# Performance work log

Hardware: AMD Instinct MI355X
Metric: run time of the kernel (lower is better)

Reference implementation:

```python
import jax, jax.numpy as jnp
import numpy as np

B, S, E, H = 2, 2048, 1024, 16
DH = E // H  # 64


def setup_inputs() -> dict:
    key = jax.random.key(0)
    ks = jax.random.split(key, 9)
    scale = 1.0 / np.sqrt(E)
    q = jax.random.normal(ks[0], (B, S, E), jnp.float32)
    k = jax.random.normal(ks[1], (B, S, E), jnp.float32)
    v = jax.random.normal(ks[2], (B, S, E), jnp.float32)
    Wq = jax.random.uniform(ks[3], (E, E), jnp.float32, -scale, scale)
    Wk = jax.random.uniform(ks[4], (E, E), jnp.float32, -scale, scale)
    Wv = jax.random.uniform(ks[5], (E, E), jnp.float32, -scale, scale)
    bq = jax.random.uniform(ks[6], (E,), jnp.float32, -scale, scale)
    bk = jax.random.uniform(ks[7], (E,), jnp.float32, -scale, scale)
    bv = jax.random.uniform(ks[8], (E,), jnp.float32, -scale, scale)
    # causal mask: True = masked. [b, s_q, s_k]
    causal = jnp.triu(jnp.ones((S, S), bool), k=1)
    mask = jnp.broadcast_to(causal, (B, S, S))
    return {"q": q, "k": k, "v": v, "Wq": Wq, "bq": bq, "Wk": Wk,
            "bk": bk, "Wv": Wv, "bv": bv, "mask": mask}


def reference(q, k, v, Wq, bq, Wk, bk, Wv, bv, mask):
    b, s_q, _ = q.shape
    s_k = k.shape[1]
    # NB: faithful to the original: .view(b, heads, s, -1) (no transpose)
    Q = (q @ Wq + bq).reshape(b, H, s_q, DH)
    K = (k @ Wk + bk).reshape(b, H, s_k, DH)
    V = (v @ Wv + bv).reshape(b, H, s_k, DH)
    scores = jnp.einsum('bhqd,bhkd->bhqk', Q, K) / jnp.sqrt(
        jnp.asarray(DH, Q.dtype))
    scores = jnp.where(mask[:, None, :, :], -jnp.inf, scores)
    attn = jax.nn.softmax(scores, axis=-1)
    out = jnp.einsum('bhqk,bhkd->bhqd', attn, V).reshape(b, s_q, -1)
    return out  # dropout p=0 / eval mode -> identity
```

## Files before the change

kernel.cpp:

```cpp
#include <hip/hip_runtime.h>

typedef unsigned short u16;
typedef __attribute__((ext_vector_type(8))) __bf16 bf16x8;
typedef __attribute__((ext_vector_type(4))) __bf16 bf16x4;
typedef __attribute__((ext_vector_type(4))) float f32x4;

#define MFMA(a, b, c) __builtin_amdgcn_mfma_f32_16x16x32_bf16((a), (b), (c), 0, 0, 0)
#define KSCALE 0.18033688011112042f

__device__ __forceinline__ void load_lds16(const void* g, void* l) {
  __builtin_amdgcn_global_load_lds(
      (__attribute__((address_space(1))) void*)(g),
      (__attribute__((address_space(3))) void*)(l), 16, 0, 0);
}

__device__ __forceinline__ float launder(float x, float lim) {
  return fminf(fmaxf(x, -lim), lim);
}

__global__ __launch_bounds__(256) void prep(
    const float* __restrict__ x0, const float* __restrict__ x1,
    const float* __restrict__ x2, const float* __restrict__ W0,
    const float* __restrict__ W1, const float* __restrict__ W2,
    __bf16* __restrict__ Xb, __bf16* __restrict__ WT) {
  __shared__ __bf16 tile[64][65];
  int bx = blockIdx.x;
  int t = threadIdx.x;
  if (bx < 3072) {
    int z = bx >> 10, blk = bx & 1023;
    const float* x = z == 0 ? x0 : (z == 1 ? x1 : x2);
    __bf16* o = Xb + (size_t)z * 4194304;
#pragma unroll
    for (int i = 0; i < 4; ++i) {
      size_t e = ((size_t)i * 262144 + (size_t)blk * 256 + t) * 4;
      f32x4 v = *(const f32x4*)&x[e];
      bf16x4 b = {(__bf16)v[0], (__bf16)v[1], (__bf16)v[2], (__bf16)v[3]};
      *(bf16x4*)&o[e] = b;
    }
  } else {
    int idx = bx - 3072;
    int z = idx >> 8, rest = idx & 255;
    const float* W = z == 0 ? W0 : (z == 1 ? W1 : W2);
    float sc = z == 0 ? KSCALE : 1.0f;
    __bf16* out = WT + (size_t)z * 1048576;
    int r0 = (rest >> 4) * 64, c0 = (rest & 15) * 64;
#pragma unroll
    for (int it = 0; it < 16; ++it) {
      int flat = it * 256 + t, r = flat >> 6, c = flat & 63;
      tile[c][r] = (__bf16)(W[(size_t)(r0 + r) * 1024 + c0 + c] * sc);
    }
    __syncthreads();
#pragma unroll
    for (int it = 0; it < 16; ++it) {
      int flat = it * 256 + t, r = flat >> 6, c = flat & 63;
      out[(size_t)(c0 + r) * 1024 + r0 + c] = tile[r][c];
    }
  }
}

__device__ __forceinline__ void pg_stage(
    const __bf16* __restrict__ A, const __bf16* __restrict__ Bm, int k0,
    __bf16* As, __bf16* Bs, int tid) {
#pragma unroll
  for (int r = 0; r < 2; ++r) {
    int flat = r * 256 + tid;
    load_lds16(A + (size_t)(flat >> 2) * 1024 + k0 + (flat & 3) * 8, &As[flat * 8]);
  }
#pragma unroll
  for (int r = 0; r < 2; ++r) {
    int flat = r * 256 + tid;
    load_lds16(Bm + (size_t)(flat >> 2) * 1024 + k0 + (flat & 3) * 8, &Bs[flat * 8]);
  }
}

__global__ __launch_bounds__(256, 3) void proj_gemm(
    const __bf16* __restrict__ Xb, const __bf16* __restrict__ WT,
    const float* __restrict__ bq, const float* __restrict__ bk,
    const float* __restrict__ bv, __bf16* __restrict__ QKV) {
  __shared__ __attribute__((aligned(16))) __bf16 As[2][4096];
  __shared__ __attribute__((aligned(16))) __bf16 Bs[2][4096];

  int tid = threadIdx.x;
  int lane = tid & 63, quad = lane >> 4, l16 = lane & 15;
  int w = tid >> 6;
  int wm = (w >> 1) * 64, wn = (w & 1) * 64;
  int m0 = blockIdx.x * 128;
  int z = m0 >> 12;
  int n0 = blockIdx.y * 128;
  const __bf16* A = Xb + (size_t)m0 * 1024;
  const __bf16* Bm = WT + (size_t)z * 1048576 + (size_t)n0 * 1024;

  f32x4 zero4 = {0.f, 0.f, 0.f, 0.f};
  f32x4 acc[4][4];
#pragma unroll
  for (int i = 0; i < 4; ++i)
#pragma unroll
    for (int j = 0; j < 4; ++j) acc[i][j] = zero4;

  pg_stage(A, Bm, 0, As[0], Bs[0], tid);

  for (int i = 0; i < 32; ++i) {
    int cur = i & 1;
    if (i < 31) {
      pg_stage(A, Bm, (i + 1) * 32, As[cur ^ 1], Bs[cur ^ 1], tid);
      asm volatile("s_waitcnt vmcnt(4)" ::: "memory");
    } else {
      asm volatile("s_waitcnt vmcnt(0)" ::: "memory");
    }
    __builtin_amdgcn_sched_barrier(0);
    __builtin_amdgcn_s_barrier();
    __builtin_amdgcn_sched_barrier(0);

    bf16x8 a[4], b[4];
#pragma unroll
    for (int mf = 0; mf < 4; ++mf)
      a[mf] = *(const bf16x8*)&As[cur][(wm + mf * 16 + l16) * 32 + quad * 8];
#pragma unroll
    for (int nf = 0; nf < 4; ++nf)
      b[nf] = *(const bf16x8*)&Bs[cur][(wn + nf * 16 + l16) * 32 + quad * 8];
#pragma unroll
    for (int mf = 0; mf < 4; ++mf)
#pragma unroll
      for (int nf = 0; nf < 4; ++nf) acc[mf][nf] = MFMA(a[mf], b[nf], acc[mf][nf]);

    __builtin_amdgcn_sched_barrier(0);
    __builtin_amdgcn_s_barrier();
    __builtin_amdgcn_sched_barrier(0);
  }

  int mrow = m0 & 4095;
  const float* bp = z == 0 ? bq : (z == 1 ? bk : bv);
  float bsc = z == 0 ? KSCALE : 1.0f;
  __bf16* O = QKV + (size_t)z * 4194304;
#pragma unroll
  for (int nf = 0; nf < 4; ++nf) {
    int n = n0 + wn + nf * 16 + l16;
    float bb = bp[n] * bsc;
#pragma unroll
    for (int mf = 0; mf < 4; ++mf) {
#pragma unroll
      for (int r = 0; r < 4; ++r) {
        int m = mrow + wm + mf * 16 + quad * 4 + r;
        O[(size_t)m * 1024 + n] = (__bf16)launder(acc[mf][nf][r] + bb, 512.f);
      }
    }
  }
}

__global__ __launch_bounds__(256) void transpose_v(
    const u16* __restrict__ Vp, u16* __restrict__ Vt) {
  int bh = blockIdx.y, s0 = blockIdx.x * 64;
  __shared__ u16 tile[64][65];
  int t = threadIdx.x;
  const u16* src = Vp + (size_t)bh * 131072;
  u16* dst = Vt + (size_t)bh * 131072;
#pragma unroll
  for (int it = 0; it < 16; ++it) {
    int flat = it * 256 + t, r = flat >> 6, d = flat & 63;
    tile[d][r] = src[(size_t)(s0 + r) * 64 + d];
  }
  __syncthreads();
#pragma unroll
  for (int it = 0; it < 16; ++it) {
    int flat = it * 256 + t, d = flat >> 6, c = flat & 63;
    dst[(size_t)d * 2048 + s0 + c] = tile[d][c];
  }
}

__global__ __launch_bounds__(256, 2) void flash_attn(
    const __bf16* __restrict__ Qp, const __bf16* __restrict__ Kp,
    const __bf16* __restrict__ Vt, float* __restrict__ out) {
  int qtA = blockIdx.x;
  int qtB = 31 - qtA;
  int bh = blockIdx.y;
  int t = threadIdx.x;
  int lane = t & 63, quad = lane >> 4, l16 = lane & 15;
  int w = t >> 6;
  int jmaxA = qtA >> 1, jmaxB = qtB >> 1;
  int sw = (l16 >> 1) & 3;

  __shared__ __attribute__((aligned(16))) __bf16 Ks[2][8192];
  __shared__ __attribute__((aligned(16))) __bf16 Vs[2][8192];
  __shared__ __attribute__((aligned(16))) __bf16 Ps[4][2048];

  const __bf16* Qb = Qp + (size_t)bh * 131072;
  const __bf16* Kb = Kp + (size_t)bh * 131072;
  const __bf16* Vb = Vt + (size_t)bh * 131072;
  __bf16* Pw = Ps[w];

  int qbA = qtA * 64 + w * 16, qbB = qtB * 64 + w * 16;

  bf16x8 qfA[2], qfB[2], ones;
#pragma unroll
  for (int i = 0; i < 8; ++i) ones[i] = (__bf16)1.0f;
#pragma unroll
  for (int kk = 0; kk < 2; ++kk) {
    qfA[kk] = *(const bf16x8*)&Qb[(size_t)(qbA + l16) * 64 + kk * 32 + quad * 8];
    qfB[kk] = *(const bf16x8*)&Qb[(size_t)(qbB + l16) * 64 + kk * 32 + quad * 8];
  }

  f32x4 zero4 = {0.f, 0.f, 0.f, 0.f};
  f32x4 oA[4], oB[4], lAacc = zero4, lBacc = zero4;
#pragma unroll
  for (int nd = 0; nd < 4; ++nd) { oA[nd] = zero4; oB[nd] = zero4; }

  int ks_kpos[4], ks_off[4], vs_d[4], vs_off[4], vs_kq[4];
#pragma unroll
  for (int p = 0; p < 4; ++p) {
    int c = p * 256 + t;
    int swz = ((c & 3) ^ ((c >> 3) & 3)) * 8;
    ks_kpos[p] = (c & 511) >> 2;
    ks_off[p] = (c >> 9) * 32 + swz;
    vs_kq[p] = c >> 8;
    vs_d[p] = (c & 255) >> 2;
    vs_off[p] = swz;
  }

  bf16x8 pk[4], pv[4];
#pragma unroll
  for (int p = 0; p < 4; ++p) {
    pk[p] = *(const bf16x8*)&Kb[(size_t)ks_kpos[p] * 64 + ks_off[p]];
    pv[p] = *(const bf16x8*)&Vb[(size_t)vs_d[p] * 2048 + vs_kq[p] * 32 + vs_off[p]];
  }
#pragma unroll
  for (int p = 0; p < 4; ++p) {
    int c = p * 256 + t;
    *(bf16x8*)&Ks[0][c * 8] = pk[p];
    *(bf16x8*)&Vs[0][c * 8] = pv[p];
  }
  if (jmaxB > 0) {
#pragma unroll
    for (int p = 0; p < 4; ++p) {
      pk[p] = *(const bf16x8*)&Kb[(size_t)(128 + ks_kpos[p]) * 64 + ks_off[p]];
      pv[p] = *(const bf16x8*)&Vb[(size_t)vs_d[p] * 2048 + 128 + vs_kq[p] * 32 + vs_off[p]];
    }
  }
  __syncthreads();

  for (int j = 0; j <= jmaxB; ++j) {
    int cur = j & 1, nxt = cur ^ 1;
    bool doA = (j <= jmaxA);

    if (j < jmaxB) {
#pragma unroll
      for (int p = 0; p < 4; ++p) {
        int c = p * 256 + t;
        *(bf16x8*)&Ks[nxt][c * 8] = pk[p];
        *(bf16x8*)&Vs[nxt][c * 8] = pv[p];
      }
      if (j + 1 < jmaxB) {
        int jn = (j + 2) * 128;
#pragma unroll
        for (int p = 0; p < 4; ++p) {
          pk[p] = *(const bf16x8*)&Kb[(size_t)(jn + ks_kpos[p]) * 64 + ks_off[p]];
          pv[p] = *(const bf16x8*)&Vb[(size_t)vs_d[p] * 2048 + jn + vs_kq[p] * 32 + vs_off[p]];
        }
      }
    }

    f32x4 sA[8], sB[8];
#pragma unroll
    for (int nt = 0; nt < 8; ++nt) {
      bf16x8 k0 = *(const bf16x8*)&Ks[cur][(nt * 16 + l16) * 32 + (quad ^ sw) * 8];
      bf16x8 k1 = *(const bf16x8*)&Ks[cur][4096 + (nt * 16 + l16) * 32 + (quad ^ sw) * 8];
      f32x4 zb = zero4;
      zb = MFMA(k0, qfB[0], zb);
      zb = MFMA(k1, qfB[1], zb);
      sB[nt] = zb;
      if (doA) {
        f32x4 za = zero4;
        za = MFMA(k0, qfA[0], za);
        za = MFMA(k1, qfA[1], za);
        sA[nt] = za;
      }
    }

    if (j == jmaxB) {
      int qg = qbB + l16;
#pragma unroll
      for (int nt = 0; nt < 8; ++nt) {
        int kg = j * 128 + nt * 16 + quad * 4;
#pragma unroll
        for (int r = 0; r < 4; ++r)
          if (kg + r > qg) sB[nt][r] = -1e30f;
      }
    }
#pragma unroll
    for (int nt = 0; nt < 8; ++nt) {
      bf16x4 pb;
#pragma unroll
      for (int r = 0; r < 4; ++r)
        pb[r] = (__bf16)__builtin_amdgcn_exp2f(sB[nt][r]);
      *(bf16x4*)&Pw[l16 * 128 + (((nt * 4 + quad) ^ (l16 * 2)) & 31) * 4] = pb;
    }
    {
      bf16x8 pf[4];
#pragma unroll
      for (int kk = 0; kk < 4; ++kk)
        pf[kk] = *(const bf16x8*)&Pw[l16 * 128 + (((kk * 8 + quad * 2) ^ (l16 * 2)) & 31) * 4];
#pragma unroll
      for (int kk = 0; kk < 4; ++kk) {
        lBacc = MFMA(ones, pf[kk], lBacc);
#pragma unroll
        for (int nd = 0; nd < 4; ++nd) {
          bf16x8 av = *(const bf16x8*)&Vs[cur][kk * 2048 + (nd * 16 + l16) * 32 + (quad ^ sw) * 8];
          oB[nd] = MFMA(av, pf[kk], oB[nd]);
        }
      }
    }

    if (doA) {
      if (j == jmaxA) {
        int qg = qbA + l16;
#pragma unroll
        for (int nt = 0; nt < 8; ++nt) {
          int kg = j * 128 + nt * 16 + quad * 4;
#pragma unroll
          for (int r = 0; r < 4; ++r)
            if (kg + r > qg) sA[nt][r] = -1e30f;
        }
      }
#pragma unroll
      for (int nt = 0; nt < 8; ++nt) {
        bf16x4 pb;
#pragma unroll
        for (int r = 0; r < 4; ++r)
          pb[r] = (__bf16)__builtin_amdgcn_exp2f(sA[nt][r]);
        *(bf16x4*)&Pw[l16 * 128 + (((nt * 4 + quad) ^ (l16 * 2)) & 31) * 4] = pb;
      }
      bf16x8 pf[4];
#pragma unroll
      for (int kk = 0; kk < 4; ++kk)
        pf[kk] = *(const bf16x8*)&Pw[l16 * 128 + (((kk * 8 + quad * 2) ^ (l16 * 2)) & 31) * 4];
#pragma unroll
      for (int kk = 0; kk < 4; ++kk) {
        lAacc = MFMA(ones, pf[kk], lAacc);
#pragma unroll
        for (int nd = 0; nd < 4; ++nd) {
          bf16x8 av = *(const bf16x8*)&Vs[cur][kk * 2048 + (nd * 16 + l16) * 32 + (quad ^ sw) * 8];
          oA[nd] = MFMA(av, pf[kk], oA[nd]);
        }
      }
    }
    __syncthreads();
  }

  {
    float invA = 1.f / lAacc[0], invB = 1.f / lBacc[0];
    int qA = qbA + l16, qB = qbB + l16;
#pragma unroll
    for (int nd = 0; nd < 4; ++nd) {
      f32x4 a, b;
#pragma unroll
      for (int r = 0; r < 4; ++r) {
        a[r] = launder(oA[nd][r] * invA, 512.f);
        b[r] = launder(oB[nd][r] * invB, 512.f);
      }
      *(f32x4*)&out[(size_t)bh * 131072 + (size_t)qA * 64 + nd * 16 + quad * 4] = a;
      *(f32x4*)&out[(size_t)bh * 131072 + (size_t)qB * 64 + nd * 16 + quad * 4] = b;
    }
  }
}

extern "C" void kernel_launch(void* const* d_in, const int* in_sizes, int n_in,
                              void* d_out, int out_size, void* d_ws, size_t ws_size,
                              hipStream_t stream) {
  (void)in_sizes; (void)n_in; (void)out_size; (void)ws_size;
  const float* q  = (const float*)d_in[0];
  const float* k  = (const float*)d_in[1];
  const float* v  = (const float*)d_in[2];
  const float* Wq = (const float*)d_in[3];
  const float* bq = (const float*)d_in[4];
  const float* Wk = (const float*)d_in[5];
  const float* bk = (const float*)d_in[6];
  const float* Wv = (const float*)d_in[7];
  const float* bv = (const float*)d_in[8];

  __bf16* ws  = (__bf16*)d_ws;
  __bf16* WT  = ws;
  __bf16* QKV = ws + (size_t)3 * 1048576;
  __bf16* Qp  = QKV;
  __bf16* Kp  = QKV + (size_t)4194304;
  __bf16* Vp  = QKV + (size_t)2 * 4194304;
  __bf16* Xb  = QKV + (size_t)3 * 4194304;
  __bf16* Vtr = Xb;

  prep<<<dim3(3840), 256, 0, stream>>>(q, k, v, Wq, Wk, Wv, Xb, WT);
  proj_gemm<<<dim3(96, 8), 256, 0, stream>>>(Xb, WT, bq, bk, bv, QKV);
  transpose_v<<<dim3(32, 32), 256, 0, stream>>>((const u16*)Vp, (u16*)Vtr);
  flash_attn<<<dim3(16, 32), 256, 0, stream>>>(Qp, Kp, Vtr, (float*)d_out);
}
```

Measured before the change: 210.5 us.

## Split paired-tile flash attention into single 64-row tiles with 64-key blocks

The flash attention kernel stops pairing two query tiles per block for causal load balancing. Each block now handles one 64-row query tile with 64-key KV blocks, on a grid of 32x32 blocks with a permuted tile order. Shared memory per block is halved and launch bounds are raised to allow 4 blocks per CU. This aims for higher occupancy and more blocks in flight, at the cost of more per-block overhead, more barriers per unit of work, and relying on the hardware scheduler for causal load balance.

```diff
diff --git a/kernel.cpp b/kernel.cpp
--- a/kernel.cpp
+++ b/kernel.cpp
@@ -167,197 +167,150 @@
   }
 }
 
-__global__ __launch_bounds__(256, 2) void flash_attn(
+__global__ __launch_bounds__(256, 4) void flash_attn(
     const __bf16* __restrict__ Qp, const __bf16* __restrict__ Kp,
     const __bf16* __restrict__ Vt, float* __restrict__ out) {
-  int qtA = blockIdx.x;
-  int qtB = 31 - qtA;
-  int bh = blockIdx.y;
+  int bh = blockIdx.x;
+  int yy = blockIdx.y;
+  int qt = (yy & 24) | (((yy >> 3) & 1) ? (7 - (yy & 7)) : (yy & 7));
+  int jmax = qt;
   int t = threadIdx.x;
   int lane = t & 63, quad = lane >> 4, l16 = lane & 15;
   int w = t >> 6;
-  int jmaxA = qtA >> 1, jmaxB = qtB >> 1;
   int sw = (l16 >> 1) & 3;
 
-  __shared__ __attribute__((aligned(16))) __bf16 Ks[2][8192];
-  __shared__ __attribute__((aligned(16))) __bf16 Vs[2][8192];
-  __shared__ __attribute__((aligned(16))) __bf16 Ps[4][2048];
+  __shared__ __attribute__((aligned(16))) __bf16 Ks[2][4096];
+  __shared__ __attribute__((aligned(16))) __bf16 Vs[2][4096];
+  __shared__ __attribute__((aligned(16))) __bf16 Ps[4][1024];
 
   const __bf16* Qb = Qp + (size_t)bh * 131072;
   const __bf16* Kb = Kp + (size_t)bh * 131072;
   const __bf16* Vb = Vt + (size_t)bh * 131072;
   __bf16* Pw = Ps[w];
 
-  int qbA = qtA * 64 + w * 16, qbB = qtB * 64 + w * 16;
-
-  bf16x8 qfA[2], qfB[2], ones;
+  int qb = qt * 64 + w * 16;
+
+  bf16x8 qf[2], ones;
 #pragma unroll
   for (int i = 0; i < 8; ++i) ones[i] = (__bf16)1.0f;
 #pragma unroll
-  for (int kk = 0; kk < 2; ++kk) {
-    qfA[kk] = *(const bf16x8*)&Qb[(size_t)(qbA + l16) * 64 + kk * 32 + quad * 8];
-    qfB[kk] = *(const bf16x8*)&Qb[(size_t)(qbB + l16) * 64 + kk * 32 + quad * 8];
-  }
+  for (int kk = 0; kk < 2; ++kk)
+    qf[kk] = *(const bf16x8*)&Qb[(size_t)(qb + l16) * 64 + kk * 32 + quad * 8];
 
   f32x4 zero4 = {0.f, 0.f, 0.f, 0.f};
-  f32x4 oA[4], oB[4], lAacc = zero4, lBacc = zero4;
-#pragma unroll
-  for (int nd = 0; nd < 4; ++nd) { oA[nd] = zero4; oB[nd] = zero4; }
-
-  int ks_kpos[4], ks_off[4], vs_d[4], vs_off[4], vs_kq[4];
-#pragma unroll
-  for (int p = 0; p < 4; ++p) {
+  f32x4 o[4], lacc = zero4;
+#pragma unroll
+  for (int nd = 0; nd < 4; ++nd) o[nd] = zero4;
+
+  int kq_row[2], kq_off[2], v_d[2], v_off[2], v_kk[2];
+#pragma unroll
+  for (int p = 0; p < 2; ++p) {
     int c = p * 256 + t;
     int swz = ((c & 3) ^ ((c >> 3) & 3)) * 8;
-    ks_kpos[p] = (c & 511) >> 2;
-    ks_off[p] = (c >> 9) * 32 + swz;
-    vs_kq[p] = c >> 8;
-    vs_d[p] = (c & 255) >> 2;
-    vs_off[p] = swz;
-  }
-
-  bf16x8 pk[4], pv[4];
-#pragma unroll
-  for (int p = 0; p < 4; ++p) {
-    pk[p] = *(const bf16x8*)&Kb[(size_t)ks_kpos[p] * 64 + ks_off[p]];
-    pv[p] = *(const bf16x8*)&Vb[(size_t)vs_d[p] * 2048 + vs_kq[p] * 32 + vs_off[p]];
-  }
-#pragma unroll
-  for (int p = 0; p < 4; ++p) {
+    kq_row[p] = (c & 255) >> 2;
+    kq_off[p] = (c >> 8) * 32 + swz;
+    v_kk[p] = c >> 8;
+    v_d[p] = (c & 255) >> 2;
+    v_off[p] = swz;
+  }
+
+  bf16x8 pk[2], pv[2];
+#pragma unroll
+  for (int p = 0; p < 2; ++p) {
+    pk[p] = *(const bf16x8*)&Kb[(size_t)kq_row[p] * 64 + kq_off[p]];
+    pv[p] = *(const bf16x8*)&Vb[(size_t)v_d[p] * 2048 + v_kk[p] * 32 + v_off[p]];
+  }
+#pragma unroll
+  for (int p = 0; p < 2; ++p) {
     int c = p * 256 + t;
     *(bf16x8*)&Ks[0][c * 8] = pk[p];
     *(bf16x8*)&Vs[0][c * 8] = pv[p];
   }
-  if (jmaxB > 0) {
-#pragma unroll
-    for (int p = 0; p < 4; ++p) {
-      pk[p] = *(const bf16x8*)&Kb[(size_t)(128 + ks_kpos[p]) * 64 + ks_off[p]];
-      pv[p] = *(const bf16x8*)&Vb[(size_t)vs_d[p] * 2048 + 128 + vs_kq[p] * 32 + vs_off[p]];
+  if (jmax > 0) {
+#pragma unroll
+    for (int p = 0; p < 2; ++p) {
+      pk[p] = *(const bf16x8*)&Kb[(size_t)(64 + kq_row[p]) * 64 + kq_off[p]];
+      pv[p] = *(const bf16x8*)&Vb[(size_t)v_d[p] * 2048 + 64 + v_kk[p] * 32 + v_off[p]];
     }
   }
   __syncthreads();
 
-  for (int j = 0; j <= jmaxB; ++j) {
+  for (int j = 0; j <= jmax; ++j) {
     int cur = j & 1, nxt = cur ^ 1;
-    bool doA = (j <= jmaxA);
-
-    if (j < jmaxB) {
-#pragma unroll
-      for (int p = 0; p < 4; ++p) {
+
+    if (j < jmax) {
+#pragma unroll
+      for (int p = 0; p < 2; ++p) {
         int c = p * 256 + t;
         *(bf16x8*)&Ks[nxt][c * 8] = pk[p];
         *(bf16x8*)&Vs[nxt][c * 8] = pv[p];
       }
-      if (j + 1 < jmaxB) {
-        int jn = (j + 2) * 128;
-#pragma unroll
-        for (int p = 0; p < 4; ++p) {
-          pk[p] = *(const bf16x8*)&Kb[(size_t)(jn + ks_kpos[p]) * 64 + ks_off[p]];
-          pv[p] = *(const bf16x8*)&Vb[(size_t)vs_d[p] * 2048 + jn + vs_kq[p] * 32 + vs_off[p]];
+      if (j + 1 < jmax) {
+        int jn = (j + 2) * 64;
+#pragma unroll
+        for (int p = 0; p < 2; ++p) {
+          pk[p] = *(const bf16x8*)&Kb[(size_t)(jn + kq_row[p]) * 64 + kq_off[p]];
+          pv[p] = *(const bf16x8*)&Vb[(size_t)v_d[p] * 2048 + jn + v_kk[p] * 32 + v_off[p]];
         }
       }
     }
 
-    f32x4 sA[8], sB[8];
-#pragma unroll
-    for (int nt = 0; nt < 8; ++nt) {
+    f32x4 s[4];
+#pragma unroll
+    for (int nt = 0; nt < 4; ++nt) {
       bf16x8 k0 = *(const bf16x8*)&Ks[cur][(nt * 16 + l16) * 32 + (quad ^ sw) * 8];
-      bf16x8 k1 = *(const bf16x8*)&Ks[cur][4096 + (nt * 16 + l16) * 32 + (quad ^ sw) * 8];
-      f32x4 zb = zero4;
-      zb = MFMA(k0, qfB[0], zb);
-      zb = MFMA(k1, qfB[1], zb);
-      sB[nt] = zb;
-      if (doA) {
-        f32x4 za = zero4;
-        za = MFMA(k0, qfA[0], za);
-        za = MFMA(k1, qfA[1], za);
-        sA[nt] = za;
-      }
-    }
-
-    if (j == jmaxB) {
-      int qg = qbB + l16;
-#pragma unroll
-      for (int nt = 0; nt < 8; ++nt) {
-        int kg = j * 128 + nt * 16 + quad * 4;
+      bf16x8 k1 = *(const bf16x8*)&Ks[cur][2048 + (nt * 16 + l16) * 32 + (quad ^ sw) * 8];
+      f32x4 z = zero4;
+      z = MFMA(k0, qf[0], z);
+      z = MFMA(k1, qf[1], z);
+      s[nt] = z;
+    }
+
+    if (j == jmax) {
+      int qg = qb + l16;
+#pragma unroll
+      for (int nt = 0; nt < 4; ++nt) {
+        int kg = j * 64 + nt * 16 + quad * 4;
 #pragma unroll
         for (int r = 0; r < 4; ++r)
-          if (kg + r > qg) sB[nt][r] = -1e30f;
-      }
-    }
-#pragma unroll
-    for (int nt = 0; nt < 8; ++nt) {
+          if (kg + r > qg) s[nt][r] = -1e30f;
+      }
+    }
+#pragma unroll
+    for (int nt = 0; nt < 4; ++nt) {
       bf16x4 pb;
 #pragma unroll
       for (int r = 0; r < 4; ++r)
-        pb[r] = (__bf16)__builtin_amdgcn_exp2f(sB[nt][r]);
-      *(bf16x4*)&Pw[l16 * 128 + (((nt * 4 + quad) ^ (l16 * 2)) & 31) * 4] = pb;
+        pb[r] = (__bf16)__builtin_amdgcn_exp2f(s[nt][r]);
+      *(bf16x4*)&Pw[l16 * 64 + (((nt * 4 + quad) ^ (l16 * 2)) & 15) * 4] = pb;
     }
     {
-      bf16x8 pf[4];
-#pragma unroll
-      for (int kk = 0; kk < 4; ++kk)
-        pf[kk] = *(const bf16x8*)&Pw[l16 * 128 + (((kk * 8 + quad * 2) ^ (l16 * 2)) & 31) * 4];
-#pragma unroll
-      for (int kk = 0; kk < 4; ++kk) {
-        lBacc = MFMA(ones, pf[kk], lBacc);
+      bf16x8 pf[2];
+#pragma unroll
+      for (int kk = 0; kk < 2; ++kk)
+        pf[kk] = *(const bf16x8*)&Pw[l16 * 64 + (((kk * 8 + quad * 2) ^ (l16 * 2)) & 15) * 4];
+#pragma unroll
+      for (int kk = 0; kk < 2; ++kk) {
+        lacc = MFMA(ones, pf[kk], lacc);
 #pragma unroll
         for (int nd = 0; nd < 4; ++nd) {
           bf16x8 av = *(const bf16x8*)&Vs[cur][kk * 2048 + (nd * 16 + l16) * 32 + (quad ^ sw) * 8];
-          oB[nd] = MFMA(av, pf[kk], oB[nd]);
+          o[nd] = MFMA(av, pf[kk], o[nd]);
         }
       }
     }
-
-    if (doA) {
-      if (j == jmaxA) {
-        int qg = qbA + l16;
-#pragma unroll
-        for (int nt = 0; nt < 8; ++nt) {
-          int kg = j * 128 + nt * 16 + quad * 4;
-#pragma unroll
-          for (int r = 0; r < 4; ++r)
-            if (kg + r > qg) sA[nt][r] = -1e30f;
-        }
-      }
-#pragma unroll
-      for (int nt = 0; nt < 8; ++nt) {
-        bf16x4 pb;
-#pragma unroll
-        for (int r = 0; r < 4; ++r)
-          pb[r] = (__bf16)__builtin_amdgcn_exp2f(sA[nt][r]);
-        *(bf16x4*)&Pw[l16 * 128 + (((nt * 4 + quad) ^ (l16 * 2)) & 31) * 4] = pb;
-      }
-      bf16x8 pf[4];
-#pragma unroll
-      for (int kk = 0; kk < 4; ++kk)
-        pf[kk] = *(const bf16x8*)&Pw[l16 * 128 + (((kk * 8 + quad * 2) ^ (l16 * 2)) & 31) * 4];
-#pragma unroll
-      for (int kk = 0; kk < 4; ++kk) {
-        lAacc = MFMA(ones, pf[kk], lAacc);
-#pragma unroll
-        for (int nd = 0; nd < 4; ++nd) {
-          bf16x8 av = *(const bf16x8*)&Vs[cur][kk * 2048 + (nd * 16 + l16) * 32 + (quad ^ sw) * 8];
-          oA[nd] = MFMA(av, pf[kk], oA[nd]);
-        }
-      }
-    }
     __syncthreads();
   }
 
   {
-    float invA = 1.f / lAacc[0], invB = 1.f / lBacc[0];
-    int qA = qbA + l16, qB = qbB + l16;
+    float inv = 1.f / lacc[0];
+    int qg = qb + l16;
 #pragma unroll
     for (int nd = 0; nd < 4; ++nd) {
-      f32x4 a, b;
-#pragma unroll
-      for (int r = 0; r < 4; ++r) {
-        a[r] = launder(oA[nd][r] * invA, 512.f);
-        b[r] = launder(oB[nd][r] * invB, 512.f);
-      }
-      *(f32x4*)&out[(size_t)bh * 131072 + (size_t)qA * 64 + nd * 16 + quad * 4] = a;
-      *(f32x4*)&out[(size_t)bh * 131072 + (size_t)qB * 64 + nd * 16 + quad * 4] = b;
+      f32x4 a;
+#pragma unroll
+      for (int r = 0; r < 4; ++r) a[r] = launder(o[nd][r] * inv, 512.f);
+      *(f32x4*)&out[(size_t)bh * 131072 + (size_t)qg * 64 + nd * 16 + quad * 4] = a;
     }
   }
 }
@@ -388,5 +341,5 @@
   prep<<<dim3(3840), 256, 0, stream>>>(q, k, v, Wq, Wk, Wv, Xb, WT);
   proj_gemm<<<dim3(96, 8), 256, 0, stream>>>(Xb, WT, bq, bk, bv, QKV);
   transpose_v<<<dim3(32, 32), 256, 0, stream>>>((const u16*)Vp, (u16*)Vtr);
-  flash_attn<<<dim3(16, 32), 256, 0, stream>>>(Qp, Kp, Vtr, (float*)d_out);
-}
+  flash_attn<<<dim3(32, 32), 256, 0, stream>>>(Qp, Kp, Vtr, (float*)d_out);
+}
```

New measurement: 204.8 us. 1.03x faster.
